# Kernel optimization log

Hardware: AMD Instinct MI355X
Metric: run time of the kernel (lower is better)

Reference implementation:

```python
import jax, jax.numpy as jnp
import numpy as np


def _gru(x, h, Wih, Whh, bih, bhh):
    # torch.nn.GRUCell math. x:(1,in), h:(1,H), Wih:(3H,in), Whh:(3H,H)
    gi = x @ Wih.T + bih
    gh = h @ Whh.T + bhh
    i_r, i_z, i_n = jnp.split(gi, 3, axis=-1)
    h_r, h_z, h_n = jnp.split(gh, 3, axis=-1)
    r = jax.nn.sigmoid(i_r + h_r)
    z = jax.nn.sigmoid(i_z + h_z)
    n = jnp.tanh(i_n + r * h_n)
    return (1.0 - z) * n + z * h


def _combine(S, Wa, ba, va):
    # SelfAttention.combine: additive attention over the stack axis.
    # S:(k,1,H), Wa:(H,A), ba:(A,), va:(A,)
    e = jnp.tanh(S @ Wa + ba) @ va          # (k,1) energies
    w = jax.nn.softmax(e, axis=0)            # softmax over stacked hidden states
    return jnp.sum(w[..., None] * S, axis=0)  # (1,H)


def setup_inputs() -> dict:
    key = jax.random.key(0)
    ks = jax.random.split(key, 20)
    T, F, H, A, L = 16384, 2048, 16, 64, 6
    G = 3 * H
    s = 0.1  # weight scale for numerical sanity
    return {
        "batch": jax.random.normal(ks[0], (T, 1, F), jnp.float32),
        "h0": jax.random.normal(ks[1], (L, 1, H), jnp.float32),
        "W_ih0": jax.random.normal(ks[2], (G, F), jnp.float32) * s,
        "W_hh0": jax.random.normal(ks[3], (G, H), jnp.float32) * s,
        "b_ih0": jax.random.normal(ks[4], (G,), jnp.float32) * s,
        "b_hh0": jax.random.normal(ks[5], (G,), jnp.float32) * s,
        "W_ih": jax.random.normal(ks[6], (L - 1, G, H), jnp.float32) * s,
        "W_hh": jax.random.normal(ks[7], (L - 1, G, H), jnp.float32) * s,
        "b_ih": jax.random.normal(ks[8], (L - 1, G), jnp.float32) * s,
        "b_hh": jax.random.normal(ks[9], (L - 1, G), jnp.float32) * s,
        "Wa": jax.random.normal(ks[10], (L, H, A), jnp.float32) * s,
        "ba": jax.random.normal(ks[11], (L, A), jnp.float32) * s,
        "va": jax.random.normal(ks[12], (L, A), jnp.float32) * s,
        "fc1_w": jax.random.normal(ks[13], (32, H), jnp.float32) * s,
        "fc1_b": jax.random.normal(ks[14], (32,), jnp.float32) * s,
        "fc2_w": jax.random.normal(ks[15], (1, 32), jnp.float32) * s,
        "fc2_b": jax.random.normal(ks[16], (1,), jnp.float32) * s,
    }


def reference(batch, h0, W_ih0, W_hh0, b_ih0, b_hh0, W_ih, W_hh, b_ih, b_hh,
              Wa, ba, va, fc1_w, fc1_b, fc2_w, fc2_b):
    L = Wa.shape[0]

    def step(h_s, x):
        # h_s: (L,1,H) carried hidden states, x: (1,F) current token
        inp = x.reshape(1, -1)
        new = []
        for l in range(L):
            if l == 0:
                inp = _gru(inp, h_s[0], W_ih0, W_hh0, b_ih0, b_hh0)
            else:
                inp = _gru(inp, h_s[l], W_ih[l - 1], W_hh[l - 1], b_ih[l - 1], b_hh[l - 1])
            new.append(inp)
        newS = jnp.stack(new)  # (L,1,H)
        # layer i attends over hidden states of layers i..L-1 (feedback combine)
        h_next = jnp.stack([_combine(newS[i:], Wa[i], ba[i], va[i]) for i in range(L)])
        top = h_next[-1].reshape(-1)  # (H,); dropout is identity in eval mode
        out = (top @ fc1_w.T + fc1_b) @ fc2_w.T + fc2_b  # (1,)
        return h_next, out

    _, outs = jax.lax.scan(step, h0, batch)
    return outs  # (T,1)
```

## Files before the change

### kernel.cpp

```cpp
#include <hip/hip_runtime.h>
#include <cstdint>
#include <cstddef>


#define TT 16384
#define FF 2048
#define HH 16
#define LL 6
#define GG 48
#define CHUNK 64
#define LOG2E 1.44269504088896340736f

__device__ float g_gi0p[(TT + CHUNK) * 64];

__device__ __forceinline__ float exp2_(float x) { return __builtin_amdgcn_exp2f(x); }
__device__ __forceinline__ float rcp_(float x) { return __builtin_amdgcn_rcpf(x); }
__device__ __forceinline__ float sig_n(float s) { return rcp_(1.f + exp2_(s)); }
__device__ __forceinline__ float tanh_p(float s) { return fmaf(-2.f, rcp_(exp2_(s) + 1.f), 1.f); }

#define MEMBAR() __asm__ __volatile__("" ::: "memory")

__device__ __forceinline__ float rdlane(float v, int l) {
  union { float f; int i; } a, b;
  a.f = v; b.i = __builtin_amdgcn_readlane(a.i, l); return b.f;
}
template <int CTRL>
__device__ __forceinline__ float dppf(float v) {
  union { float f; int i; } a, b;
  a.f = v; b.i = __builtin_amdgcn_mov_dpp(a.i, CTRL, 0xF, 0xF, true); return b.f;
}
template <int Q>
__device__ __forceinline__ float qbcast(float v) { return dppf<Q | (Q << 2) | (Q << 4) | (Q << 6)>(v); }

__device__ __forceinline__ float rowsum16(float v) {
  v += dppf<0xB1>(v);
  v += dppf<0x4E>(v);
  v += dppf<0x141>(v);
  v += dppf<0x140>(v);
  return v;
}
__device__ __forceinline__ float dot16r(const float (&w)[16], const float (&h)[16]) {
  float s0 = w[0] * h[0], s1 = w[1] * h[1], s2 = w[2] * h[2], s3 = w[3] * h[3];
#pragma unroll
  for (int k = 4; k < 16; k += 4) {
    s0 = fmaf(w[k], h[k], s0);       s1 = fmaf(w[k + 1], h[k + 1], s1);
    s2 = fmaf(w[k + 2], h[k + 2], s2); s3 = fmaf(w[k + 3], h[k + 3], s3);
  }
  return (s0 + s1) + (s2 + s3);
}
__device__ __forceinline__ float dot16i(const float (&w)[16], const float (&h)[16], float init) {
  float s0 = fmaf(w[0], h[0], init), s1 = w[1] * h[1], s2 = w[2] * h[2], s3 = w[3] * h[3];
#pragma unroll
  for (int k = 4; k < 16; k += 4) {
    s0 = fmaf(w[k], h[k], s0);       s1 = fmaf(w[k + 1], h[k + 1], s1);
    s2 = fmaf(w[k + 2], h[k + 2], s2); s3 = fmaf(w[k + 3], h[k + 3], s3);
  }
  return (s0 + s1) + (s2 + s3);
}

__device__ __forceinline__ int ldAcq(int* f) {
  return __hip_atomic_load(f, __ATOMIC_ACQUIRE, __HIP_MEMORY_SCOPE_WORKGROUP);
}
__device__ __forceinline__ void pollGE(int* f, int target) {
  while (ldAcq(f) < target) {}
}
__device__ __forceinline__ void waitFlag(int* f, int& cache, int need) {
  if (cache < need) { do { cache = ldAcq(f); } while (cache < need); }
}
__device__ __forceinline__ void sigRel(int* f, int v) {
  __hip_atomic_store(f, v, __ATOMIC_RELAXED, __HIP_MEMORY_SCOPE_WORKGROUP);
}

__device__ __forceinline__ void combBlock(const float4 A0, const float4 A1, const float4 A2,
                                          const float4 A3, float nsv,
                                          const float (&Wa)[16], float ba, float va,
                                          const float (&Wh)[16],
                                          float& S, float& ha, float& Pa) {
  float nr[16] = {A0.x, A0.y, A0.z, A0.w, A1.x, A1.y, A1.z, A1.w,
                  A2.x, A2.y, A2.z, A2.w, A3.x, A3.y, A3.z, A3.w};
  float u = dot16i(Wa, nr, ba);
  float P = dot16r(Wh, nr);
  float pe = va * tanh_p(u);
  float r = rowsum16(pe);
  float e = (rdlane(r, 0) + rdlane(r, 16)) + (rdlane(r, 32) + rdlane(r, 48));
  float w = exp2_(e);
  S += w; ha = fmaf(w, nsv, ha); Pa = fmaf(w, P, Pa);
}

__global__ __launch_bounds__(256) void gi0_gemm(const float* __restrict__ X,
                                                const float* __restrict__ W,
                                                const float* __restrict__ bias) {
  __shared__ float xs[64][132];
  __shared__ float ws[48][132];
  const int tid = threadIdx.x;
  const int t0 = blockIdx.x * 64;
  const int tg = tid & 15;
  const int tt = tid >> 4;
  float acc[4][3];
#pragma unroll
  for (int u = 0; u < 4; ++u)
#pragma unroll
    for (int v = 0; v < 3; ++v) acc[u][v] = 0.f;

  for (int k0 = 0; k0 < FF; k0 += 128) {
#pragma unroll
    for (int i = 0; i < 32; ++i) {
      int e = tid + 256 * i; int r = e >> 7, c = e & 127;
      xs[r][c] = X[(size_t)(t0 + r) * FF + k0 + c];
    }
#pragma unroll
    for (int i = 0; i < 24; ++i) {
      int e = tid + 256 * i; int r = e >> 7, c = e & 127;
      ws[r][c] = W[(size_t)r * FF + k0 + c];
    }
    __syncthreads();
#pragma unroll 8
    for (int c = 0; c < 128; ++c) {
      float x0 = xs[tt][c], x1 = xs[tt + 16][c], x2 = xs[tt + 32][c], x3 = xs[tt + 48][c];
      float w0 = ws[tg][c], w1 = ws[tg + 16][c], w2 = ws[tg + 32][c];
      acc[0][0] += x0 * w0; acc[0][1] += x0 * w1; acc[0][2] += x0 * w2;
      acc[1][0] += x1 * w0; acc[1][1] += x1 * w1; acc[1][2] += x1 * w2;
      acc[2][0] += x2 * w0; acc[2][1] += x2 * w1; acc[2][2] += x2 * w2;
      acc[3][0] += x3 * w0; acc[3][1] += x3 * w1; acc[3][2] += x3 * w2;
    }
    __syncthreads();
  }
  const float gsc3[3] = {-LOG2E, -LOG2E, 2.f * LOG2E};
#pragma unroll
  for (int u = 0; u < 4; ++u)
#pragma unroll
    for (int v = 0; v < 3; ++v)
      g_gi0p[(size_t)(t0 + tt + 16 * u) * 64 + tg * 4 + v] =
          (acc[u][v] + bias[tg + 16 * v]) * gsc3[v];
}

__global__ __launch_bounds__(512, 1) void fbrnn_scan(
    const float* __restrict__ h0,
    const float* __restrict__ Whh0, const float* __restrict__ bhh0,
    const float* __restrict__ Wih, const float* __restrict__ Whh,
    const float* __restrict__ bih, const float* __restrict__ bhh,
    const float* __restrict__ Wa, const float* __restrict__ ba,
    const float* __restrict__ va,
    const float* __restrict__ fc1w, const float* __restrict__ fc1b,
    const float* __restrict__ fc2w, const float* __restrict__ fc2b,
    float* __restrict__ out) {
  __shared__ __align__(16) float nsS[2][LL * HH];
  __shared__ __align__(16) float4 recS[5 * 64];
  __shared__ __align__(16) float4 partS[4 * 64];
  __shared__ __align__(16) float nsOut[256 * HH];
  __shared__ __align__(16) float chunkS[2][CHUNK * 64];
  __shared__ int flagNs;
  __shared__ int flagChunk;
  __shared__ int flagOut;
  __shared__ int gen5[2];

  const int tid = threadIdx.x;
  const int wv = tid >> 6;
  const int lane = tid & 63;
  const int qg = lane & 3;
  const int kk = lane >> 2;
  const int gate = (qg < 3 ? qg : 2);
  const int G = gate * 16 + kk;
  const float gsc = (gate == 2) ? 2.f * LOG2E : -LOG2E;

  const bool isChain = (wv == 0);
  const bool isStream = (wv == 4);
  const bool isFc = (wv == 6);
  const int hRow = (wv == 6 || wv == 1) ? 0 : (wv == 2 || wv == 5) ? 1 : -1;
  const int pRow = (wv == 3) ? 2 : (wv == 7) ? 3 : (wv == 5) ? 4 : -1;
  const int pSlot = (wv == 6) ? 0 : (wv == 1) ? 1 : (wv == 2) ? 2 : (wv == 5) ? 3 : -1;

  float WBih[5][16];
  float WB5[16];  float bhh5R = 0.f;
  float Wa0R[16], Wh0R[16], Wa1R[16], Wh1R[16];
  float ba0R = 0.f, va0R = 0.f, bb0 = 0.f;
  float ba1R = 0.f, va1R = 0.f, bb1 = 0.f;
  float WaP[16], WhP[16];
  float baP = 0.f, vaP = 0.f, bhhP = 0.f;
  float WaH[16], WhH[16];
  float baH = 0.f, vaH = 0.f;
  float fc1R[16];
  float fb1 = 0.f, fw2 = 0.f, fb2 = 0.f;

  if (isChain) {
#pragma unroll
    for (int l = 0; l < 5; ++l)
#pragma unroll
      for (int k = 0; k < 16; ++k) WBih[l][k] = Wih[((l * GG) + G) * 16 + k] * gsc;
#pragma unroll
    for (int k = 0; k < 16; ++k) WB5[k] = Whh[(4 * GG + G) * 16 + k] * gsc;
    bhh5R = (bhh[4 * GG + G] + bih[4 * GG + G]) * gsc;
#pragma unroll
    for (int k = 0; k < 16; ++k) {
      Wa0R[k] = Wa[(0 * 16 + k) * 64 + lane] * (2.f * LOG2E);
      Wa1R[k] = Wa[(1 * 16 + k) * 64 + lane] * (2.f * LOG2E);
      Wh0R[k] = Whh0[G * 16 + k] * gsc;
      Wh1R[k] = Whh[(0 * GG + G) * 16 + k] * gsc;
    }
    ba0R = ba[0 * 64 + lane] * (2.f * LOG2E); va0R = va[0 * 64 + lane] * LOG2E;
    ba1R = ba[1 * 64 + lane] * (2.f * LOG2E); va1R = va[1 * 64 + lane] * LOG2E;
    bb0 = bhh0[G] * gsc;
    bb1 = (bhh[0 * GG + G] + bih[0 * GG + G]) * gsc;
  }
  if (pRow >= 0) {
#pragma unroll
    for (int k = 0; k < 16; ++k) WaP[k] = Wa[(pRow * 16 + k) * 64 + lane] * (2.f * LOG2E);
    baP = ba[pRow * 64 + lane] * (2.f * LOG2E);
    vaP = va[pRow * 64 + lane] * LOG2E;
    const float* ws = Whh + ((pRow - 1) * GG + G) * 16;
#pragma unroll
    for (int k = 0; k < 16; ++k) WhP[k] = ws[k] * gsc;
    bhhP = (bhh[(pRow - 1) * GG + G] + bih[(pRow - 1) * GG + G]) * gsc;
  }
  if (hRow >= 0) {
#pragma unroll
    for (int k = 0; k < 16; ++k) WaH[k] = Wa[(hRow * 16 + k) * 64 + lane] * (2.f * LOG2E);
    baH = ba[hRow * 64 + lane] * (2.f * LOG2E);
    vaH = va[hRow * 64 + lane] * LOG2E;
    const float* ws = (hRow == 0) ? (Whh0 + G * 16) : (Whh + ((hRow - 1) * GG + G) * 16);
#pragma unroll
    for (int k = 0; k < 16; ++k) WhH[k] = ws[k] * gsc;
  }
  if (isFc) {
    const int m = lane & 31;
#pragma unroll
    for (int k = 0; k < 16; ++k) fc1R[k] = fc1w[m * 16 + k];
    fb1 = fc1b[m]; fw2 = fc2w[m]; fb2 = fc2b[0];
  }

  if (tid == 0) { flagNs = 0; flagChunk = 1; flagOut = 0; gen5[0] = 0; gen5[1] = 0; }

  float hv5 = 0.f, gh5reg = 0.f;
  float gh0n = 0.f, hv0n = 0.f, gh1n = 0.f, hv1n = 0.f;
  if (isChain) {
    float hr[16];
#pragma unroll
    for (int k = 0; k < 16; ++k) hr[k] = h0[5 * 16 + k];
    hv5 = h0[5 * 16 + kk];
    gh5reg = dot16i(WB5, hr, bhh5R);
#pragma unroll
    for (int k = 0; k < 16; ++k) hr[k] = h0[0 * 16 + k];
    hv0n = h0[0 * 16 + kk];
    gh0n = dot16i(Wh0R, hr, bb0);
#pragma unroll
    for (int k = 0; k < 16; ++k) hr[k] = h0[1 * 16 + k];
    hv1n = h0[1 * 16 + kk];
    gh1n = dot16i(Wh1R, hr, bb1);
  } else if (pRow >= 0) {
    float hr[16];
#pragma unroll
    for (int k = 0; k < 16; ++k) hr[k] = h0[pRow * 16 + k];
    float4 rr;
    rr.x = dot16i(WhP, hr, bhhP);
    rr.y = h0[pRow * 16 + kk];
    rr.z = __int_as_float(0);
    rr.w = 0.f;
    recS[pRow * 64 + lane] = rr;
  }
  if (isStream) {
    const float4* src = (const float4*)g_gi0p;
    float4* dst = (float4*)(&chunkS[0][0]);
#pragma unroll
    for (int q = 0; q < 16; ++q) dst[q * 64 + lane] = src[q * 64 + lane];
  }
  if (pSlot >= 0) partS[pSlot * 64 + lane] = make_float4(0.f, 0.f, 0.f, __int_as_float(0));
  __syncthreads();

#define EBLOCK(J, WaX, baX, vaX, WhX, Sx, hax, Pax) do {                          \
    waitFlag(&flagNs, fcache, t * 8 + (J) + 1);                                   \
    const float4* np_ = (const float4*)&nsS[nb][(J) * 16];                        \
    float4 A0_ = np_[0], A1_ = np_[1], A2_ = np_[2], A3_ = np_[3];                \
    float nsv_ = nsS[nb][(J) * 16 + kk];                                          \
    combBlock(A0_, A1_, A2_, A3_, nsv_, WaX, baX, vaX, WhX, Sx, hax, Pax);        \
  } while (0)

#define TAILFIN(ROW, Sv, hav, Pav) do {                                           \
    float4 A0, A1, A2, A3; float nsv5;                                            \
    for (;;) {                                                                    \
      int g5 = ldAcq(&gen5[nb]);                                                  \
      MEMBAR();                                                                   \
      const float4* np = (const float4*)&nsS[nb][5 * 16];                         \
      A0 = np[0]; A1 = np[1]; A2 = np[2]; A3 = np[3];                             \
      nsv5 = nsS[nb][5 * 16 + kk];                                                \
      MEMBAR();                                                                   \
      if (g5 >= tgt) break;                                                       \
    }                                                                             \
    combBlock(A0, A1, A2, A3, nsv5, WaP, baP, vaP, WhP, Sv, hav, Pav);            \
    const float inv_ = rcp_(Sv);                                                  \
    float4 rr_; rr_.x = fmaf(Pav, inv_, bhhP); rr_.y = hav * inv_;                \
    rr_.z = __int_as_float(tgt); rr_.w = 0.f;                                     \
    recS[(ROW) * 64 + lane] = rr_;                                                \
  } while (0)

  if (isStream) {
#pragma unroll 1
    for (int c = 1; c < 256; ++c) {
      if (c >= 2) pollGE(&flagNs, ((c - 1) * 64 - 1) * 8 + 1);
      const float4* src = (const float4*)(g_gi0p + ((size_t)c << 12));
      float4* dst = (float4*)(&chunkS[c & 1][0]);
#pragma unroll
      for (int q = 0; q < 16; ++q) dst[q * 64 + lane] = src[q * 64 + lane];
      MEMBAR();
      sigRel(&flagChunk, c + 1);
    }
    return;
  }

  if (isFc) {
    int fcache = 0;
#pragma unroll 1
    for (int t = 0; t < TT; ++t) {
      const int nb = t & 1;
      float Sh = 0.f, hah = 0.f, Pah = 0.f;
      EBLOCK(0, WaH, baH, vaH, WhH, Sh, hah, Pah);
      EBLOCK(1, WaH, baH, vaH, WhH, Sh, hah, Pah);
      EBLOCK(2, WaH, baH, vaH, WhH, Sh, hah, Pah);
      partS[0 * 64 + lane] = make_float4(Sh, hah, Pah, __int_as_float(t + 1));
      waitFlag(&flagNs, fcache, t * 8 + 6);
      const float4* np = (const float4*)(nsOut + (t & 255) * 16);
      float4 a0 = np[0], a1 = np[1], a2 = np[2], a3 = np[3];
      float nr[16] = {a0.x, a0.y, a0.z, a0.w, a1.x, a1.y, a1.z, a1.w,
                      a2.x, a2.y, a2.z, a2.w, a3.x, a3.y, a3.z, a3.w};
      float y = dot16i(fc1R, nr, fb1);
      float p = rowsum16(y * fw2);
      float o = rdlane(p, 0) + rdlane(p, 16) + fb2;
      if (lane == 0) out[t] = o;
      MEMBAR();
      sigRel(&flagOut, t + 1);
    }
    return;
  }

  if (!isChain) {
    int fcache = 0;
    if (wv == 1) {
#pragma unroll 1
      for (int t = 0; t < TT; ++t) {
        const int nb = t & 1;
        float Sh = 0.f, hah = 0.f, Pah = 0.f;
        EBLOCK(3, WaH, baH, vaH, WhH, Sh, hah, Pah);
        EBLOCK(4, WaH, baH, vaH, WhH, Sh, hah, Pah);
        partS[1 * 64 + lane] = make_float4(Sh, hah, Pah, __int_as_float(t + 1));
      }
    } else if (wv == 2) {
#pragma unroll 1
      for (int t = 0; t < TT; ++t) {
        const int nb = t & 1;
        float Sh = 0.f, hah = 0.f, Pah = 0.f;
        EBLOCK(1, WaH, baH, vaH, WhH, Sh, hah, Pah);
        EBLOCK(2, WaH, baH, vaH, WhH, Sh, hah, Pah);
        EBLOCK(3, WaH, baH, vaH, WhH, Sh, hah, Pah);
        partS[2 * 64 + lane] = make_float4(Sh, hah, Pah, __int_as_float(t + 1));
      }
    } else if (wv == 5) {
#pragma unroll 1
      for (int t = 0; t < TT; ++t) {
        const int nb = t & 1;
        const int tgt = t + 1;
        float Sh = 0.f, hah = 0.f, Pah = 0.f;
        EBLOCK(4, WaH, baH, vaH, WhH, Sh, hah, Pah);
        partS[3 * 64 + lane] = make_float4(Sh, hah, Pah, __int_as_float(tgt));
        float S = 0.f, ha = 0.f, Pa = 0.f;
        EBLOCK(4, WaP, baP, vaP, WhP, S, ha, Pa);
        TAILFIN(4, S, ha, Pa);
      }
    } else if (wv == 3) {
#pragma unroll 1
      for (int t = 0; t < TT; ++t) {
        const int nb = t & 1;
        const int tgt = t + 1;
        float S = 0.f, ha = 0.f, Pa = 0.f;
        EBLOCK(2, WaP, baP, vaP, WhP, S, ha, Pa);
        EBLOCK(3, WaP, baP, vaP, WhP, S, ha, Pa);
        EBLOCK(4, WaP, baP, vaP, WhP, S, ha, Pa);
        TAILFIN(2, S, ha, Pa);
      }
    } else {
#pragma unroll 1
      for (int t = 0; t < TT; ++t) {
        const int nb = t & 1;
        const int tgt = t + 1;
        float S = 0.f, ha = 0.f, Pa = 0.f;
        EBLOCK(3, WaP, baP, vaP, WhP, S, ha, Pa);
        EBLOCK(4, WaP, baP, vaP, WhP, S, ha, Pa);
        TAILFIN(3, S, ha, Pa);
      }
    }
    return;
  }

  float gnext = chunkS[0][lane];
  float ns_sg[16];
#pragma unroll 1
  for (int t = 0; t < TT; ++t) {
    const int wb = t & 1;

    float ghv[6], hv[6];
    ghv[0] = gh0n; hv[0] = hv0n;
    ghv[1] = gh1n; hv[1] = hv1n;
    ghv[5] = gh5reg; hv[5] = hv5;
    float4 r2, r3, r4;
    float gpre = 0.f;
    float gi0v = gnext;
    float ns = 0.f;
#pragma unroll
    for (int l = 0; l < 6; ++l) {
      if (l == 2) {
        if (!((__float_as_int(r2.z) >= t) & (__float_as_int(r3.z) >= t) &
              (__float_as_int(r4.z) >= t))) {
          do {
            MEMBAR();
            r2 = recS[2 * 64 + lane]; r3 = recS[3 * 64 + lane]; r4 = recS[4 * 64 + lane];
            MEMBAR();
          } while (!((__float_as_int(r2.z) >= t) & (__float_as_int(r3.z) >= t) &
                     (__float_as_int(r4.z) >= t)));
        }
        ghv[2] = r2.x; hv[2] = r2.y;
        ghv[3] = r3.x; hv[3] = r3.y;
        ghv[4] = r4.x; hv[4] = r4.y;
      }
      const float gh_g = ghv[l];
      const float s = (l == 0) ? (gi0v + gh_g) : dot16i(WBih[l - 1], ns_sg, gh_g);
      const float sg = sig_n(s);
      const float smg = s - gh_g;
      const float sr = qbcast<0>(sg);
      const float sz = qbcast<1>(sg);
      const float a = sz * hv[l];
      const float b = 1.f - sz;
      const float tq = tanh_p(fmaf(sr, gh_g, smg));
      ns = fmaf(tq, b, a);
      if (qg == 2) {
        nsS[wb][l * 16 + kk] = ns;
        if (l == 5) nsOut[(t & 255) * 16 + kk] = ns;
      }
      MEMBAR();
      if (l == 5 && lane == 0) { sigRel(&gen5[wb], t + 1); sigRel(&flagNs, t * 8 + 6); }
#pragma unroll
      for (int k = 0; k < 16; ++k) ns_sg[k] = rdlane(ns, 4 * k + 2);
      if (l < 5 && lane == 0) sigRel(&flagNs, t * 8 + l + 1);
      if (l == 0) {
        if ((t & 63) == 63) {
          const int cn = (t + 1) >> 6;
          if (cn < 256) pollGE(&flagChunk, cn + 1);
        }
        if ((t & 63) == 32) pollGE(&flagOut, t - 64);
        gpre = chunkS[((t + 1) >> 6) & 1][((t + 1) & 63) * 64 + lane];
        MEMBAR();
        r2 = recS[2 * 64 + lane]; r3 = recS[3 * 64 + lane]; r4 = recS[4 * 64 + lane];
        MEMBAR();
      }
    }
    const float hv5n = qbcast<2>(ns);
    gh5reg = dot16i(WB5, ns_sg, bhh5R);
    float u0 = dot16i(Wa0R, ns_sg, ba0R);
    float u1 = dot16i(Wa1R, ns_sg, ba1R);
    float P0 = dot16r(Wh0R, ns_sg);
    float P1 = dot16r(Wh1R, ns_sg);
    MEMBAR();
    float4 p0a = partS[0 * 64 + lane], p0b = partS[1 * 64 + lane];
    float4 p1a = partS[2 * 64 + lane], p1b = partS[3 * 64 + lane];
    MEMBAR();
    float pe0 = va0R * tanh_p(u0);
    float pe1 = va1R * tanh_p(u1);
    float rs0 = rowsum16(pe0);
    float rs1 = rowsum16(pe1);
    float e0 = (rdlane(rs0, 0) + rdlane(rs0, 16)) + (rdlane(rs0, 32) + rdlane(rs0, 48));
    float e1 = (rdlane(rs1, 0) + rdlane(rs1, 16)) + (rdlane(rs1, 32) + rdlane(rs1, 48));
    float wj0 = exp2_(e0), wj1 = exp2_(e1);
    const int tp = t + 1;
    if (!((__float_as_int(p0a.w) >= tp) & (__float_as_int(p0b.w) >= tp) &
          (__float_as_int(p1a.w) >= tp) & (__float_as_int(p1b.w) >= tp))) {
      do {
        MEMBAR();
        p0a = partS[0 * 64 + lane]; p0b = partS[1 * 64 + lane];
        p1a = partS[2 * 64 + lane]; p1b = partS[3 * 64 + lane];
        MEMBAR();
      } while (!((__float_as_int(p0a.w) >= tp) & (__float_as_int(p0b.w) >= tp) &
                 (__float_as_int(p1a.w) >= tp) & (__float_as_int(p1b.w) >= tp)));
    }
    float S0 = p0a.x + p0b.x + wj0;
    float hT0 = p0a.y + p0b.y + wj0 * hv5n;
    float PT0 = p0a.z + p0b.z + wj0 * P0;
    float S1 = p1a.x + p1b.x + wj1;
    float hT1 = p1a.y + p1b.y + wj1 * hv5n;
    float PT1 = p1a.z + p1b.z + wj1 * P1;
    const float inv0 = rcp_(S0);
    const float inv1 = rcp_(S1);
    gh0n = fmaf(PT0, inv0, bb0); hv0n = hT0 * inv0;
    gh1n = fmaf(PT1, inv1, bb1); hv1n = hT1 * inv1;
    hv5 = hv5n;
    gnext = gpre;
  }
}

extern "C" void kernel_launch(void* const* d_in, const int* in_sizes, int n_in,
                              void* d_out, int out_size, void* d_ws, size_t ws_size,
                              hipStream_t stream) {
  const float* batch = (const float*)d_in[0];
  const float* h0    = (const float*)d_in[1];
  const float* Wih0  = (const float*)d_in[2];
  const float* Whh0  = (const float*)d_in[3];
  const float* bih0  = (const float*)d_in[4];
  const float* bhh0  = (const float*)d_in[5];
  const float* Wih   = (const float*)d_in[6];
  const float* Whh   = (const float*)d_in[7];
  const float* bih   = (const float*)d_in[8];
  const float* bhh   = (const float*)d_in[9];
  const float* Wa    = (const float*)d_in[10];
  const float* ba    = (const float*)d_in[11];
  const float* va    = (const float*)d_in[12];
  const float* fc1w  = (const float*)d_in[13];
  const float* fc1b  = (const float*)d_in[14];
  const float* fc2w  = (const float*)d_in[15];
  const float* fc2b  = (const float*)d_in[16];
  float* out = (float*)d_out;
  (void)in_sizes; (void)n_in; (void)out_size; (void)d_ws; (void)ws_size;

  gi0_gemm<<<TT / 64, 256, 0, stream>>>(batch, Wih0, bih0);
  fbrnn_scan<<<1, 512, 0, stream>>>(h0, Whh0, bhh0, Wih, Whh, bih, bhh,
                                    Wa, ba, va, fc1w, fc1b, fc2w, fc2b, out);
}
```

Before: 22.11 ms.

## Move layer 3-4 attention partials into chain wave and rework GRU update

Helper wave 1 is retired. Wave 2 now covers only layers 1-2, and wave 5 now does only the row-4 tail. The chain wave computes the attention contributions of layers 3 and 4 for rows 0 and 1 inline, right after producing those layers, so it waits on two partial slots instead of four. The GRU output update is rewritten algebraically around h-1, folding tanh and the (1-z) blend into one exp/rcp/fma sequence with fewer ops on the serial path. The cost is extra dot products and reductions on the critical chain wave, in exchange for less cross-wave synchronisation.

Result: slower. 27.54 ms (+24.6%).

```diff
diff --git a/kernel.cpp b/kernel.cpp
--- a/kernel.cpp
+++ b/kernel.cpp
@@ -166,9 +166,10 @@
   const bool isChain = (wv == 0);
   const bool isStream = (wv == 4);
   const bool isFc = (wv == 6);
-  const int hRow = (wv == 6 || wv == 1) ? 0 : (wv == 2 || wv == 5) ? 1 : -1;
+  const bool isIdle = (wv == 1);
+  const int hRow = (wv == 6) ? 0 : (wv == 2) ? 1 : -1;
   const int pRow = (wv == 3) ? 2 : (wv == 7) ? 3 : (wv == 5) ? 4 : -1;
-  const int pSlot = (wv == 6) ? 0 : (wv == 1) ? 1 : (wv == 2) ? 2 : (wv == 5) ? 3 : -1;
+  const int pSlot = (wv == 6) ? 0 : (wv == 2) ? 2 : -1;
 
   float WBih[5][16];
   float WB5[16];  float bhh5R = 0.f;
@@ -230,21 +231,21 @@
 
   if (tid == 0) { flagNs = 0; flagChunk = 1; flagOut = 0; gen5[0] = 0; gen5[1] = 0; }
 
-  float hv5 = 0.f, gh5reg = 0.f;
-  float gh0n = 0.f, hv0n = 0.f, gh1n = 0.f, hv1n = 0.f;
+  float hv5m = 0.f, gh5reg = 0.f;
+  float gh0n = 0.f, hv0m = 0.f, gh1n = 0.f, hv1m = 0.f;
   if (isChain) {
     float hr[16];
 #pragma unroll
     for (int k = 0; k < 16; ++k) hr[k] = h0[5 * 16 + k];
-    hv5 = h0[5 * 16 + kk];
+    hv5m = h0[5 * 16 + kk] - 1.f;
     gh5reg = dot16i(WB5, hr, bhh5R);
 #pragma unroll
     for (int k = 0; k < 16; ++k) hr[k] = h0[0 * 16 + k];
-    hv0n = h0[0 * 16 + kk];
+    hv0m = h0[0 * 16 + kk] - 1.f;
     gh0n = dot16i(Wh0R, hr, bb0);
 #pragma unroll
     for (int k = 0; k < 16; ++k) hr[k] = h0[1 * 16 + k];
-    hv1n = h0[1 * 16 + kk];
+    hv1m = h0[1 * 16 + kk] - 1.f;
     gh1n = dot16i(Wh1R, hr, bb1);
   } else if (pRow >= 0) {
     float hr[16];
@@ -252,7 +253,7 @@
     for (int k = 0; k < 16; ++k) hr[k] = h0[pRow * 16 + k];
     float4 rr;
     rr.x = dot16i(WhP, hr, bhhP);
-    rr.y = h0[pRow * 16 + kk];
+    rr.y = h0[pRow * 16 + kk] - 1.f;
     rr.z = __int_as_float(0);
     rr.w = 0.f;
     recS[pRow * 64 + lane] = rr;
@@ -265,6 +266,8 @@
   }
   if (pSlot >= 0) partS[pSlot * 64 + lane] = make_float4(0.f, 0.f, 0.f, __int_as_float(0));
   __syncthreads();
+
+  if (isIdle) return;
 
 #define EBLOCK(J, WaX, baX, vaX, WhX, Sx, hax, Pax) do {                          \
     waitFlag(&flagNs, fcache, t * 8 + (J) + 1);                                   \
@@ -287,7 +290,7 @@
     }                                                                             \
     combBlock(A0, A1, A2, A3, nsv5, WaP, baP, vaP, WhP, Sv, hav, Pav);            \
     const float inv_ = rcp_(Sv);                                                  \
-    float4 rr_; rr_.x = fmaf(Pav, inv_, bhhP); rr_.y = hav * inv_;                \
+    float4 rr_; rr_.x = fmaf(Pav, inv_, bhhP); rr_.y = fmaf(hav, inv_, -1.f);     \
     rr_.z = __int_as_float(tgt); rr_.w = 0.f;                                     \
     recS[(ROW) * 64 + lane] = rr_;                                                \
   } while (0)
@@ -315,7 +318,9 @@
       EBLOCK(0, WaH, baH, vaH, WhH, Sh, hah, Pah);
       EBLOCK(1, WaH, baH, vaH, WhH, Sh, hah, Pah);
       EBLOCK(2, WaH, baH, vaH, WhH, Sh, hah, Pah);
+      MEMBAR();
       partS[0 * 64 + lane] = make_float4(Sh, hah, Pah, __int_as_float(t + 1));
+      MEMBAR();
       waitFlag(&flagNs, fcache, t * 8 + 6);
       const float4* np = (const float4*)(nsOut + (t & 255) * 16);
       float4 a0 = np[0], a1 = np[1], a2 = np[2], a3 = np[3];
@@ -333,36 +338,16 @@
 
   if (!isChain) {
     int fcache = 0;
-    if (wv == 1) {
-#pragma unroll 1
-      for (int t = 0; t < TT; ++t) {
-        const int nb = t & 1;
-        float Sh = 0.f, hah = 0.f, Pah = 0.f;
-        EBLOCK(3, WaH, baH, vaH, WhH, Sh, hah, Pah);
-        EBLOCK(4, WaH, baH, vaH, WhH, Sh, hah, Pah);
-        partS[1 * 64 + lane] = make_float4(Sh, hah, Pah, __int_as_float(t + 1));
-      }
-    } else if (wv == 2) {
+    if (wv == 2) {
 #pragma unroll 1
       for (int t = 0; t < TT; ++t) {
         const int nb = t & 1;
         float Sh = 0.f, hah = 0.f, Pah = 0.f;
         EBLOCK(1, WaH, baH, vaH, WhH, Sh, hah, Pah);
         EBLOCK(2, WaH, baH, vaH, WhH, Sh, hah, Pah);
-        EBLOCK(3, WaH, baH, vaH, WhH, Sh, hah, Pah);
+        MEMBAR();
         partS[2 * 64 + lane] = make_float4(Sh, hah, Pah, __int_as_float(t + 1));
-      }
-    } else if (wv == 5) {
-#pragma unroll 1
-      for (int t = 0; t < TT; ++t) {
-        const int nb = t & 1;
-        const int tgt = t + 1;
-        float Sh = 0.f, hah = 0.f, Pah = 0.f;
-        EBLOCK(4, WaH, baH, vaH, WhH, Sh, hah, Pah);
-        partS[3 * 64 + lane] = make_float4(Sh, hah, Pah, __int_as_float(tgt));
-        float S = 0.f, ha = 0.f, Pa = 0.f;
-        EBLOCK(4, WaP, baP, vaP, WhP, S, ha, Pa);
-        TAILFIN(4, S, ha, Pa);
+        MEMBAR();
       }
     } else if (wv == 3) {
 #pragma unroll 1
@@ -375,7 +360,7 @@
         EBLOCK(4, WaP, baP, vaP, WhP, S, ha, Pa);
         TAILFIN(2, S, ha, Pa);
       }
-    } else {
+    } else if (wv == 7) {
 #pragma unroll 1
       for (int t = 0; t < TT; ++t) {
         const int nb = t & 1;
@@ -385,6 +370,15 @@
         EBLOCK(4, WaP, baP, vaP, WhP, S, ha, Pa);
         TAILFIN(3, S, ha, Pa);
       }
+    } else {
+#pragma unroll 1
+      for (int t = 0; t < TT; ++t) {
+        const int nb = t & 1;
+        const int tgt = t + 1;
+        float S = 0.f, ha = 0.f, Pa = 0.f;
+        EBLOCK(4, WaP, baP, vaP, WhP, S, ha, Pa);
+        TAILFIN(4, S, ha, Pa);
+      }
     }
     return;
   }
@@ -395,14 +389,16 @@
   for (int t = 0; t < TT; ++t) {
     const int wb = t & 1;
 
-    float ghv[6], hv[6];
-    ghv[0] = gh0n; hv[0] = hv0n;
-    ghv[1] = gh1n; hv[1] = hv1n;
-    ghv[5] = gh5reg; hv[5] = hv5;
+    float ghv[6], hvm1[6];
+    ghv[0] = gh0n; hvm1[0] = hv0m;
+    ghv[1] = gh1n; hvm1[1] = hv1m;
+    ghv[5] = gh5reg; hvm1[5] = hv5m;
     float4 r2, r3, r4;
     float gpre = 0.f;
     float gi0v = gnext;
     float ns = 0.f;
+    float S0a = 0.f, ha0a = 0.f, Pa0a = 0.f;
+    float S1a = 0.f, ha1a = 0.f, Pa1a = 0.f;
 #pragma unroll
     for (int l = 0; l < 6; ++l) {
       if (l == 2) {
@@ -415,9 +411,9 @@
           } while (!((__float_as_int(r2.z) >= t) & (__float_as_int(r3.z) >= t) &
                      (__float_as_int(r4.z) >= t)));
         }
-        ghv[2] = r2.x; hv[2] = r2.y;
-        ghv[3] = r3.x; hv[3] = r3.y;
-        ghv[4] = r4.x; hv[4] = r4.y;
+        ghv[2] = r2.x; hvm1[2] = r2.y;
+        ghv[3] = r3.x; hvm1[3] = r3.y;
+        ghv[4] = r4.x; hvm1[4] = r4.y;
       }
       const float gh_g = ghv[l];
       const float s = (l == 0) ? (gi0v + gh_g) : dot16i(WBih[l - 1], ns_sg, gh_g);
@@ -425,10 +421,11 @@
       const float smg = s - gh_g;
       const float sr = qbcast<0>(sg);
       const float sz = qbcast<1>(sg);
-      const float a = sz * hv[l];
-      const float b = 1.f - sz;
-      const float tq = tanh_p(fmaf(sr, gh_g, smg));
-      ns = fmaf(tq, b, a);
+      const float nb2 = fmaf(2.f, sz, -2.f);
+      const float apb = fmaf(sz, hvm1[l], 1.f);
+      const float E = exp2_(fmaf(sr, gh_g, smg));
+      const float R = rcp_(E + 1.f);
+      ns = fmaf(nb2, R, apb);
       if (qg == 2) {
         nsS[wb][l * 16 + kk] = ns;
         if (l == 5) nsOut[(t & 255) * 16 + kk] = ns;
@@ -449,17 +446,32 @@
         r2 = recS[2 * 64 + lane]; r3 = recS[3 * 64 + lane]; r4 = recS[4 * 64 + lane];
         MEMBAR();
       }
-    }
+      if (l == 3 || l == 4) {
+        const float nsq = qbcast<2>(ns);
+        float uj0 = dot16i(Wa0R, ns_sg, ba0R);
+        float uj1 = dot16i(Wa1R, ns_sg, ba1R);
+        float Pj0 = dot16r(Wh0R, ns_sg);
+        float Pj1 = dot16r(Wh1R, ns_sg);
+        float pj0 = va0R * tanh_p(uj0);
+        float pj1 = va1R * tanh_p(uj1);
+        float rj0 = rowsum16(pj0);
+        float rj1 = rowsum16(pj1);
+        float ej0 = (rdlane(rj0, 0) + rdlane(rj0, 16)) + (rdlane(rj0, 32) + rdlane(rj0, 48));
+        float ej1 = (rdlane(rj1, 0) + rdlane(rj1, 16)) + (rdlane(rj1, 32) + rdlane(rj1, 48));
+        float wj0_ = exp2_(ej0), wj1_ = exp2_(ej1);
+        S0a += wj0_; ha0a = fmaf(wj0_, nsq, ha0a); Pa0a = fmaf(wj0_, Pj0, Pa0a);
+        S1a += wj1_; ha1a = fmaf(wj1_, nsq, ha1a); Pa1a = fmaf(wj1_, Pj1, Pa1a);
+      }
+    }
+    MEMBAR();
+    float4 q0 = partS[0 * 64 + lane], q2 = partS[2 * 64 + lane];
+    MEMBAR();
     const float hv5n = qbcast<2>(ns);
     gh5reg = dot16i(WB5, ns_sg, bhh5R);
     float u0 = dot16i(Wa0R, ns_sg, ba0R);
     float u1 = dot16i(Wa1R, ns_sg, ba1R);
     float P0 = dot16r(Wh0R, ns_sg);
     float P1 = dot16r(Wh1R, ns_sg);
-    MEMBAR();
-    float4 p0a = partS[0 * 64 + lane], p0b = partS[1 * 64 + lane];
-    float4 p1a = partS[2 * 64 + lane], p1b = partS[3 * 64 + lane];
-    MEMBAR();
     float pe0 = va0R * tanh_p(u0);
     float pe1 = va1R * tanh_p(u1);
     float rs0 = rowsum16(pe0);
@@ -468,27 +480,24 @@
     float e1 = (rdlane(rs1, 0) + rdlane(rs1, 16)) + (rdlane(rs1, 32) + rdlane(rs1, 48));
     float wj0 = exp2_(e0), wj1 = exp2_(e1);
     const int tp = t + 1;
-    if (!((__float_as_int(p0a.w) >= tp) & (__float_as_int(p0b.w) >= tp) &
-          (__float_as_int(p1a.w) >= tp) & (__float_as_int(p1b.w) >= tp))) {
+    if (!((__float_as_int(q0.w) >= tp) & (__float_as_int(q2.w) >= tp))) {
       do {
         MEMBAR();
-        p0a = partS[0 * 64 + lane]; p0b = partS[1 * 64 + lane];
-        p1a = partS[2 * 64 + lane]; p1b = partS[3 * 64 + lane];
+        q0 = partS[0 * 64 + lane]; q2 = partS[2 * 64 + lane];
         MEMBAR();
-      } while (!((__float_as_int(p0a.w) >= tp) & (__float_as_int(p0b.w) >= tp) &
-                 (__float_as_int(p1a.w) >= tp) & (__float_as_int(p1b.w) >= tp)));
-    }
-    float S0 = p0a.x + p0b.x + wj0;
-    float hT0 = p0a.y + p0b.y + wj0 * hv5n;
-    float PT0 = p0a.z + p0b.z + wj0 * P0;
-    float S1 = p1a.x + p1b.x + wj1;
-    float hT1 = p1a.y + p1b.y + wj1 * hv5n;
-    float PT1 = p1a.z + p1b.z + wj1 * P1;
+      } while (!((__float_as_int(q0.w) >= tp) & (__float_as_int(q2.w) >= tp)));
+    }
+    float S0 = q0.x + S0a + wj0;
+    float hT0 = q0.y + ha0a + wj0 * hv5n;
+    float PT0 = q0.z + Pa0a + wj0 * P0;
+    float S1 = q2.x + S1a + wj1;
+    float hT1 = q2.y + ha1a + wj1 * hv5n;
+    float PT1 = q2.z + Pa1a + wj1 * P1;
     const float inv0 = rcp_(S0);
     const float inv1 = rcp_(S1);
-    gh0n = fmaf(PT0, inv0, bb0); hv0n = hT0 * inv0;
-    gh1n = fmaf(PT1, inv1, bb1); hv1n = hT1 * inv1;
-    hv5 = hv5n;
+    gh0n = fmaf(PT0, inv0, bb0); hv0m = fmaf(hT0, inv0, -1.f);
+    gh1n = fmaf(PT1, inv1, bb1); hv1m = fmaf(hT1, inv1, -1.f);
+    hv5m = hv5n - 1.f;
     gnext = gpre;
   }
 }
```
